# Kernel optimization log

Hardware: AMD Instinct MI355X
Metric: run time of the kernel (lower is better)

Reference implementation:

```python
import jax, jax.numpy as jnp
import numpy as np

B, T, F = 16384, 48, 4
UNITS = 256
OUT_STEPS = 24


def setup_inputs() -> dict:
    key = jax.random.key(0)
    ks = jax.random.split(key, 6)
    s_x = 1.0 / np.sqrt(F)
    s_h = 1.0 / np.sqrt(UNITS)
    return {
        "x": jax.random.normal(ks[0], (B, T, F), jnp.float32),
        "Wx": jax.random.normal(ks[1], (F, 4 * UNITS), jnp.float32) * s_x,
        "Wh": jax.random.normal(ks[2], (UNITS, 4 * UNITS), jnp.float32) * s_h,
        "b": jnp.zeros((4 * UNITS,), jnp.float32),
        "Wd": jax.random.normal(ks[3], (UNITS, F), jnp.float32) * s_h,
        "bd": jnp.zeros((F,), jnp.float32),
    }


def _lstm_cell(xt, h, c, Wx, Wh, b):
    # Keras LSTMCell gate order: i, f, g(cell candidate), o
    z = xt @ Wx + h @ Wh + b  # [B, 4*units]
    i, f, g, o = jnp.split(z, 4, axis=-1)
    i = jax.nn.sigmoid(i)
    f = jax.nn.sigmoid(f)
    g = jnp.tanh(g)
    o = jax.nn.sigmoid(o)
    c_new = f * c + i * g
    h_new = o * jnp.tanh(c_new)
    return h_new, c_new


def reference(x, Wx, Wh, b, Wd, bd):
    bsz = x.shape[0]
    h0 = jnp.zeros((bsz, UNITS), x.dtype)
    c0 = jnp.zeros((bsz, UNITS), x.dtype)

    # --- warmup: run LSTM over the input window, keep final state ---
    def warm_step(carry, xt):
        h, c = carry
        h, c = _lstm_cell(xt, h, c, Wx, Wh, b)
        return (h, c), None

    (h, c), _ = jax.lax.scan(warm_step, (h0, c0), jnp.swapaxes(x, 0, 1))
    pred0 = h @ Wd + bd  # first prediction [B, F]

    def ar_step(carry, _):
        h, c, pred = carry
        h, c = _lstm_cell(pred, h, c, Wx, Wh, b)
        pred = h @ Wd + bd
        return (h, c, pred), pred

    _, preds = jax.lax.scan(ar_step, (h, c, pred0), None, length=OUT_STEPS - 1)
    preds = jnp.concatenate([pred0[None], preds], axis=0)  # [out_steps, B, F]
    return jnp.swapaxes(preds, 0, 1)  # [B, out_steps, F]
```

## Files before the change

### kernel.cpp

```cpp
#include <hip/hip_runtime.h>


typedef unsigned short u16;
typedef __attribute__((ext_vector_type(8))) short bf16x8;
typedef __attribute__((ext_vector_type(4))) float f32x4;
typedef __attribute__((ext_vector_type(16))) float f32x16;

#define PITCH 296
#define HB 18944
#define WARM 48
#define STEPS 71
#define LOG2E  1.442695041f
#define LOG2E2 2.885390082f

__device__ __forceinline__ u16 f2bf(float f) {
    unsigned u = __float_as_uint(f);
    u += 0x7FFFu + ((u >> 16) & 1u);
    return (u16)(u >> 16);
}

__device__ __forceinline__ unsigned pk_bf16(float a, float b) {
    unsigned d;
    asm("v_cvt_pk_bf16_f32 %0, %1, %2" : "=v"(d) : "v"(a), "v"(b));
    return d;
}

__device__ __forceinline__ void sync_lds() {
    asm volatile("s_waitcnt lgkmcnt(0)\n\ts_barrier" ::: "memory");
}

__device__ __forceinline__ void wait4(const int* f, int tgt) {
    for (;;) {
        int a = ((volatile const int*)f)[0];
        int b = ((volatile const int*)f)[1];
        int c = ((volatile const int*)f)[2];
        int d = ((volatile const int*)f)[3];
        if (a >= tgt && b >= tgt && c >= tgt && d >= tgt) break;
    }
    asm volatile("" ::: "memory");
}

__global__ void prep_weights(const float* __restrict__ Wx,
                             const float* __restrict__ Wh,
                             const float* __restrict__ b,
                             const float* __restrict__ Wd,
                             const float* __restrict__ bd,
                             u16* __restrict__ whext,
                             u16* __restrict__ wdp) {
    int idx = blockIdx.x * 256 + threadIdx.x;
    if (idx < 34816) {
        int lane = idx & 63;
        int fr = idx >> 6;
        int g = fr & 3;
        int wv = (fr >> 2) & 7;
        int kt = fr >> 5;
        int k0 = kt * 16 + (lane >> 5) * 8;
        int n = 256 * g + 32 * wv + (lane & 31);
        float sc = (g == 2) ? LOG2E2 : LOG2E;
        u16 v[8];
#pragma unroll
        for (int j = 0; j < 8; ++j) {
            int k = k0 + j;
            float f = 0.0f;
            if (k < 256) f = Wh[k * 1024 + n];
            else if (k < 260) f = Wx[(k - 256) * 1024 + n];
            else if (k == 260) f = b[n];
            v[j] = f2bf(f * sc);
        }
        ushort4* dst = (ushort4*)(whext + (size_t)idx * 8);
        dst[0] = make_ushort4(v[0], v[1], v[2], v[3]);
        dst[1] = make_ushort4(v[4], v[5], v[6], v[7]);
    } else if (idx < 34816 + 576) {
        int id2 = idx - 34816;
        int lane = id2 & 63;
        int kc = id2 >> 6;
        int m = lane & 15;
        int k0 = kc * 32 + (lane >> 4) * 8;
        u16 v[8];
#pragma unroll
        for (int j = 0; j < 8; ++j) {
            int k = k0 + j;
            float f = 0.0f;
            if (m < 4) {
                if (k < 256) f = Wd[k * 4 + m];
                else if (k == 260) f = bd[m];
            }
            v[j] = f2bf(f);
        }
        ushort4* dst = (ushort4*)(wdp + (size_t)id2 * 8);
        dst[0] = make_ushort4(v[0], v[1], v[2], v[3]);
        dst[1] = make_ushort4(v[4], v[5], v[6], v[7]);
    }
}

#define WL(DST, T) do {                                                       \
    const char* _p = wpw + ((size_t)(T) << 15);                               \
    DST[0] = *(const bf16x8*)(_p + voffl);                                    \
    DST[1] = *(const bf16x8*)(_p + voffl + 1024);                             \
    DST[2] = *(const bf16x8*)(_p + voffl + 2048);                             \
    DST[3] = *(const bf16x8*)(_p + voffl + 3072);                             \
} while (0)

#define HL(DST, T) do {                                                       \
    DST[0] = *(const bf16x8*)&hr[hrow0 + (T) * 16];                           \
    DST[1] = *(const bf16x8*)&hr[hrow1 + (T) * 16];                           \
} while (0)

#define MT(WA, HBX)                                                           \
    _Pragma("unroll") for (int m = 0; m < 2; ++m)                             \
    _Pragma("unroll") for (int g = 0; g < 4; ++g)                             \
        acc[m][g] = __builtin_amdgcn_mfma_f32_32x32x16_bf16(                  \
            WA[g], HBX[m], acc[m][g], 0, 0, 0);

#define STG(K, AW, HBX) do { MT(AW, HBX); WL(AW, (K) + 3); HL(HBX, (K) + 2); } while (0)

__global__ __launch_bounds__(512, 2) void lstm_main(
    const float* __restrict__ x, const u16* __restrict__ whext,
    const u16* __restrict__ wdp, float* __restrict__ out) {
    __shared__ __align__(16) u16 hbuf[2 * HB];
    __shared__ int flag16[4];

    const int tid = threadIdx.x;
    const int w = tid >> 6;
    const int l = tid & 63;
    const int l31 = l & 31;
    const int lh = l >> 5;
    const long long rowBase = (long long)blockIdx.x * 64;

    {
        int4 z = make_int4(0, 0, 0, 0);
        for (int i = tid; i < 4736; i += 512) ((int4*)hbuf)[i] = z;
        if (tid < 4) flag16[tid] = 0;
    }
    sync_lds();
    if (tid < 64) {
        hbuf[tid * PITCH + 260] = (u16)0x3F80;
        hbuf[HB + tid * PITCH + 260] = (u16)0x3F80;
        const float4 xv = *(const float4*)(x + (rowBase + tid) * 192);
        uint2* p = (uint2*)&hbuf[tid * PITCH + 256];
        *p = make_uint2(pk_bf16(xv.x, xv.y), pk_bf16(xv.z, xv.w));
    }

    const char* __restrict__ wpw = (const char*)whext + (size_t)w * 4096;
    const char* __restrict__ dp = (const char*)wdp;
    const int voffl = l * 16;
    const int hrow0 = l31 * PITCH + lh * 8;
    const int hrow1 = (32 + l31) * PITCH + lh * 8;

    f32x16 c[2] = {};
    bf16x8 aw0[4], aw1[4], aw2[4];
    WL(aw0, 0);
    WL(aw1, 1);
    WL(aw2, 2);

    for (int step = 0; step < STEPS; ++step) {
        const u16* hr = hbuf + (step & 1) * HB;
        u16* hrw = hbuf + (step & 1) * HB;
        u16* hw = hbuf + ((step & 1) ^ 1) * HB;

        float4 xv = make_float4(0.f, 0.f, 0.f, 0.f);
        if (w == 0 && step < WARM - 1)
            xv = *(const float4*)(x + (rowBase + l) * 192 + (step + 1) * 4);

        sync_lds();

        if (step >= WARM && w < 4) {
            f32x4 pacc = {};
            const int col = l & 15;
            const int prow = (16 * w + col) * PITCH + (l >> 4) * 8;
#pragma unroll
            for (int kc = 0; kc < 9; ++kc) {
                bf16x8 hbp = *(const bf16x8*)&hr[prow + kc * 32];
                bf16x8 wap = *(const bf16x8*)(dp + ((size_t)kc * 64 + l) * 16);
                pacc = __builtin_amdgcn_mfma_f32_16x16x32_bf16(wap, hbp, pacc, 0, 0, 0);
            }
            if ((l >> 4) == 0) {
                int s = step - WARM;
                int batch = 16 * w + col;
                *(float4*)&out[((rowBase + batch) * 24 + s) * 4] =
                    make_float4(pacc[0], pacc[1], pacc[2], pacc[3]);
                *(uint2*)&hrw[batch * PITCH + 256] =
                    make_uint2(pk_bf16(pacc[0], pacc[1]), pk_bf16(pacc[2], pacc[3]));
            }
            asm volatile("s_waitcnt lgkmcnt(0)" ::: "memory");
            if (l == 0) *(volatile int*)&flag16[w] = step - WARM + 1;
        }

        f32x16 acc[2][4] = {};
        bf16x8 hb0[2], hb1[2];
        HL(hb0, 0);
        HL(hb1, 1);

        STG(0, aw0, hb0);
        STG(1, aw1, hb1);
#pragma unroll 1
        for (int k = 2; k < 14; k += 6) {
            STG(k + 0, aw2, hb0);
            STG(k + 1, aw0, hb1);
            STG(k + 2, aw1, hb0);
            STG(k + 3, aw2, hb1);
            STG(k + 4, aw0, hb0);
            STG(k + 5, aw1, hb1);
        }
        MT(aw2, hb0); WL(aw2, 2);
        if (step >= WARM) wait4(flag16, step - WARM + 1);
        HL(hb0, 16);
        MT(aw0, hb1); WL(aw0, 0);
        MT(aw1, hb0); WL(aw1, 1);

#pragma unroll
        for (int m = 0; m < 2; ++m) {
            const int hwrow = (32 * m + l31) * PITCH + 32 * w + 4 * lh;
#pragma unroll
            for (int q = 0; q < 4; ++q) {
                unsigned pk[2];
#pragma unroll
                for (int hp = 0; hp < 2; ++hp) {
                    float h2[2];
#pragma unroll
                    for (int rr = 0; rr < 2; ++rr) {
                        const int r = q * 4 + hp * 2 + rr;
                        float ei = __builtin_amdgcn_exp2f(-acc[m][0][r]);
                        float ef = __builtin_amdgcn_exp2f(-acc[m][1][r]);
                        float eg = __builtin_amdgcn_exp2f(-acc[m][2][r]);
                        float eo = __builtin_amdgcn_exp2f(-acc[m][3][r]);
                        float ai = 1.0f + ei, af = 1.0f + ef;
                        float ag = 1.0f + eg, ao = 1.0f + eo;
                        float P  = ai * ag;
                        float rD = __builtin_amdgcn_rcpf(P * af);
                        float cn = fmaf(c[m][r] * P, rD, (1.0f - eg) * af * rD);
                        c[m][r] = cn;
                        float ec = __builtin_amdgcn_exp2f(-LOG2E2 * cn);
                        float rE = __builtin_amdgcn_rcpf(ao * (1.0f + ec));
                        h2[rr] = (1.0f - ec) * rE;
                    }
                    pk[hp] = pk_bf16(h2[0], h2[1]);
                }
                *(uint2*)&hw[hwrow + 8 * q] = make_uint2(pk[0], pk[1]);
            }
        }

        if (step < WARM - 1) {
            if (w == 0) {
                uint2* p = (uint2*)&hw[l * PITCH + 256];
                *p = make_uint2(pk_bf16(xv.x, xv.y), pk_bf16(xv.z, xv.w));
            }
        }
    }

    sync_lds();
    if (w < 4) {
        const u16* hf = hbuf + (((STEPS - 1) & 1) ^ 1) * HB;
        f32x4 pacc = {};
        const int col = l & 15;
        const int prow = (16 * w + col) * PITCH + (l >> 4) * 8;
#pragma unroll
        for (int kc = 0; kc < 9; ++kc) {
            bf16x8 hbp = *(const bf16x8*)&hf[prow + kc * 32];
            bf16x8 wap = *(const bf16x8*)(dp + ((size_t)kc * 64 + l) * 16);
            pacc = __builtin_amdgcn_mfma_f32_16x16x32_bf16(wap, hbp, pacc, 0, 0, 0);
        }
        if ((l >> 4) == 0) {
            int batch = 16 * w + col;
            *(float4*)&out[((rowBase + batch) * 24 + 23) * 4] =
                make_float4(pacc[0], pacc[1], pacc[2], pacc[3]);
        }
    }
}

extern "C" void kernel_launch(void* const* d_in, const int* in_sizes, int n_in,
                              void* d_out, int out_size, void* d_ws, size_t ws_size,
                              hipStream_t stream) {
    const float* x  = (const float*)d_in[0];
    const float* Wx = (const float*)d_in[1];
    const float* Wh = (const float*)d_in[2];
    const float* b  = (const float*)d_in[3];
    const float* Wd = (const float*)d_in[4];
    const float* bd = (const float*)d_in[5];
    float* out = (float*)d_out;

    u16* whext = (u16*)d_ws;
    u16* wdp = (u16*)((char*)d_ws + 557056);

    prep_weights<<<(34816 + 576 + 255) / 256, 256, 0, stream>>>(Wx, Wh, b, Wd, bd, whext, wdp);
    lstm_main<<<256, 512, 0, stream>>>(x, whext, wdp, out);
}
```

Measured before the change: 742.8 us.

## Repartition LSTM gate GEMM so each wave covers one batch half and 64 units

Changes the per-wave work split in the recurrent gate GEMM. Previously each of the 8 waves computed all 64 batch rows for 32 hidden units (4 gate tiles × 2 batch tiles). Now each wave computes 32 batch rows for 64 hidden units (8 gate tiles × 1 batch tile). Weight prep is reordered to match, and weight prefetch goes from triple to double buffering with 8 fragments per stage. This halves the LDS h-fragment reads per MFMA and doubles the global/L2 weight traffic per wave, shifting the bottleneck from LDS toward weight loads. It also raises register pressure for the weight buffers.

```diff
diff --git a/kernel.cpp b/kernel.cpp
--- a/kernel.cpp
+++ b/kernel.cpp
@@ -51,11 +51,13 @@
     if (idx < 34816) {
         int lane = idx & 63;
         int fr = idx >> 6;
-        int g = fr & 3;
-        int wv = (fr >> 2) & 7;
+        int a = fr & 7;
+        int p2 = (fr >> 3) & 3;
         int kt = fr >> 5;
+        int g = a >> 1;
+        int su = a & 1;
         int k0 = kt * 16 + (lane >> 5) * 8;
-        int n = 256 * g + 32 * wv + (lane & 31);
+        int n = 256 * g + 64 * p2 + 32 * su + (lane & 31);
         float sc = (g == 2) ? LOG2E2 : LOG2E;
         u16 v[8];
 #pragma unroll
@@ -99,20 +101,21 @@
     DST[1] = *(const bf16x8*)(_p + voffl + 1024);                             \
     DST[2] = *(const bf16x8*)(_p + voffl + 2048);                             \
     DST[3] = *(const bf16x8*)(_p + voffl + 3072);                             \
+    const char* _q = _p + 4096;                                               \
+    DST[4] = *(const bf16x8*)(_q + voffl);                                    \
+    DST[5] = *(const bf16x8*)(_q + voffl + 1024);                             \
+    DST[6] = *(const bf16x8*)(_q + voffl + 2048);                             \
+    DST[7] = *(const bf16x8*)(_q + voffl + 3072);                             \
 } while (0)
 
-#define HL(DST, T) do {                                                       \
-    DST[0] = *(const bf16x8*)&hr[hrow0 + (T) * 16];                           \
-    DST[1] = *(const bf16x8*)&hr[hrow1 + (T) * 16];                           \
-} while (0)
+#define HLD(DST, T) do { DST = *(const bf16x8*)&hr[hrow + (T) * 16]; } while (0)
 
 #define MT(WA, HBX)                                                           \
-    _Pragma("unroll") for (int m = 0; m < 2; ++m)                             \
-    _Pragma("unroll") for (int g = 0; g < 4; ++g)                             \
-        acc[m][g] = __builtin_amdgcn_mfma_f32_32x32x16_bf16(                  \
-            WA[g], HBX[m], acc[m][g], 0, 0, 0);
-
-#define STG(K, AW, HBX) do { MT(AW, HBX); WL(AW, (K) + 3); HL(HBX, (K) + 2); } while (0)
+    _Pragma("unroll") for (int a = 0; a < 8; ++a)                             \
+        acc[a] = __builtin_amdgcn_mfma_f32_32x32x16_bf16(                     \
+            WA[a], HBX, acc[a], 0, 0, 0);
+
+#define STG(K, AWX, HBX) do { MT(AWX, HBX); WL(AWX, (K) + 2); HLD(HBX, (K) + 2); } while (0)
 
 __global__ __launch_bounds__(512, 2) void lstm_main(
     const float* __restrict__ x, const u16* __restrict__ whext,
@@ -122,6 +125,8 @@
 
     const int tid = threadIdx.x;
     const int w = tid >> 6;
+    const int p = w & 3;
+    const int mt = w >> 2;
     const int l = tid & 63;
     const int l31 = l & 31;
     const int lh = l >> 5;
@@ -137,21 +142,20 @@
         hbuf[tid * PITCH + 260] = (u16)0x3F80;
         hbuf[HB + tid * PITCH + 260] = (u16)0x3F80;
         const float4 xv = *(const float4*)(x + (rowBase + tid) * 192);
-        uint2* p = (uint2*)&hbuf[tid * PITCH + 256];
-        *p = make_uint2(pk_bf16(xv.x, xv.y), pk_bf16(xv.z, xv.w));
-    }
-
-    const char* __restrict__ wpw = (const char*)whext + (size_t)w * 4096;
+        uint2* q = (uint2*)&hbuf[tid * PITCH + 256];
+        *q = make_uint2(pk_bf16(xv.x, xv.y), pk_bf16(xv.z, xv.w));
+    }
+
+    const char* __restrict__ wpw = (const char*)whext + (size_t)p * 8192;
     const char* __restrict__ dp = (const char*)wdp;
     const int voffl = l * 16;
-    const int hrow0 = l31 * PITCH + lh * 8;
-    const int hrow1 = (32 + l31) * PITCH + lh * 8;
+    const int hrow = (32 * mt + l31) * PITCH + lh * 8;
 
     f32x16 c[2] = {};
-    bf16x8 aw0[4], aw1[4], aw2[4];
+    bf16x8 aw0[8], aw1[8];
+    bf16x8 hb0, hb1;
     WL(aw0, 0);
     WL(aw1, 1);
-    WL(aw2, 2);
 
     for (int step = 0; step < STEPS; ++step) {
         const u16* hr = hbuf + (step & 1) * HB;
@@ -186,31 +190,24 @@
             if (l == 0) *(volatile int*)&flag16[w] = step - WARM + 1;
         }
 
-        f32x16 acc[2][4] = {};
-        bf16x8 hb0[2], hb1[2];
-        HL(hb0, 0);
-        HL(hb1, 1);
-
-        STG(0, aw0, hb0);
-        STG(1, aw1, hb1);
+        f32x16 acc[8] = {};
+        HLD(hb0, 0);
+        HLD(hb1, 1);
+
 #pragma unroll 1
-        for (int k = 2; k < 14; k += 6) {
-            STG(k + 0, aw2, hb0);
-            STG(k + 1, aw0, hb1);
-            STG(k + 2, aw1, hb0);
-            STG(k + 3, aw2, hb1);
-            STG(k + 4, aw0, hb0);
-            STG(k + 5, aw1, hb1);
-        }
-        MT(aw2, hb0); WL(aw2, 2);
+        for (int k = 0; k < 14; k += 2) {
+            STG(k, aw0, hb0);
+            STG(k + 1, aw1, hb1);
+        }
+        MT(aw0, hb0); WL(aw0, 16);
         if (step >= WARM) wait4(flag16, step - WARM + 1);
-        HL(hb0, 16);
-        MT(aw0, hb1); WL(aw0, 0);
-        MT(aw1, hb0); WL(aw1, 1);
-
-#pragma unroll
-        for (int m = 0; m < 2; ++m) {
-            const int hwrow = (32 * m + l31) * PITCH + 32 * w + 4 * lh;
+        HLD(hb0, 16);
+        MT(aw1, hb1); WL(aw1, 1);
+        MT(aw0, hb0); WL(aw0, 0);
+
+#pragma unroll
+        for (int su = 0; su < 2; ++su) {
+            const int hwrow = (32 * mt + l31) * PITCH + 64 * p + 32 * su + 4 * lh;
 #pragma unroll
             for (int q = 0; q < 4; ++q) {
                 unsigned pk[2];
@@ -220,16 +217,16 @@
 #pragma unroll
                     for (int rr = 0; rr < 2; ++rr) {
                         const int r = q * 4 + hp * 2 + rr;
-                        float ei = __builtin_amdgcn_exp2f(-acc[m][0][r]);
-                        float ef = __builtin_amdgcn_exp2f(-acc[m][1][r]);
-                        float eg = __builtin_amdgcn_exp2f(-acc[m][2][r]);
-                        float eo = __builtin_amdgcn_exp2f(-acc[m][3][r]);
+                        float ei = __builtin_amdgcn_exp2f(-acc[0 + su][r]);
+                        float ef = __builtin_amdgcn_exp2f(-acc[2 + su][r]);
+                        float eg = __builtin_amdgcn_exp2f(-acc[4 + su][r]);
+                        float eo = __builtin_amdgcn_exp2f(-acc[6 + su][r]);
                         float ai = 1.0f + ei, af = 1.0f + ef;
                         float ag = 1.0f + eg, ao = 1.0f + eo;
                         float P  = ai * ag;
                         float rD = __builtin_amdgcn_rcpf(P * af);
-                        float cn = fmaf(c[m][r] * P, rD, (1.0f - eg) * af * rD);
-                        c[m][r] = cn;
+                        float cn = fmaf(c[su][r] * P, rD, (1.0f - eg) * af * rD);
+                        c[su][r] = cn;
                         float ec = __builtin_amdgcn_exp2f(-LOG2E2 * cn);
                         float rE = __builtin_amdgcn_rcpf(ao * (1.0f + ec));
                         h2[rr] = (1.0f - ec) * rE;
@@ -242,8 +239,8 @@
 
         if (step < WARM - 1) {
             if (w == 0) {
-                uint2* p = (uint2*)&hw[l * PITCH + 256];
-                *p = make_uint2(pk_bf16(xv.x, xv.y), pk_bf16(xv.z, xv.w));
+                uint2* q = (uint2*)&hw[l * PITCH + 256];
+                *q = make_uint2(pk_bf16(xv.x, xv.y), pk_bf16(xv.z, xv.w));
             }
         }
     }
```

After: 926.3 us. +24.7%, slower.
